# Kernel optimization log

Measured on AMD Instinct MI355X. Metric: run time of the kernel, lower is better.

## Reference

```python
import jax, jax.numpy as jnp
import numpy as np

N, E, B, F, H = 100000, 800000, 128, 128, 128
G = 5
INV_BN = np.float32(1.0 / np.sqrt(1.0 + 1e-5))  # eval BatchNorm, running_mean=0, running_var=1

_HEAD_SHAPES = [("norm_emb_g", (2*H,)), ("norm_emb_b", (2*H,)),
                ("fc1_W", (16, 2*H+1)), ("fc1_b", (16,)),
                ("bn1_g", (16,)), ("bn1_b", (16,)),
                ("fc2_W", (2, 2*H+3)), ("fc2_b", (2,)),
                ("fc3a_W", (4, 2*H+5)), ("fc3a_b", (4,)),
                ("fc3b_W", (5, 2*H+5)), ("fc3b_b", (5,)),
                ("normc_g", (2*H+5,)), ("normc_b", (2*H+5,))]


def setup_inputs() -> dict:
    key = jax.random.key(0)
    ks = jax.random.split(key, 64)
    p = lambda i, shape: jax.random.normal(ks[i], shape, jnp.float32) * 0.05
    inp = {
        "x": jax.random.normal(ks[0], (N, F), jnp.float32),
        "edge_index": jax.random.randint(ks[1], (2, E), 0, N, dtype=jnp.int32),
        "edge_direction": jax.random.randint(ks[2], (E,), 0, 2, dtype=jnp.int32),
        "batch": jnp.sort(jax.random.randint(ks[3], (N,), 0, B, dtype=jnp.int32)),
        "graph_feature": jax.random.normal(ks[4], (B, G), jnp.float32),
        "task": 1,
    }
    i = 5
    for pref in ("pre", "suc"):
        for l in range(3):
            inp[pref + "_Wl%d" % l] = p(i, (H, H)); i += 1
            inp[pref + "_bl%d" % l] = p(i, (H,)); i += 1
            inp[pref + "_Wr%d" % l] = p(i, (H, H)); i += 1
    for name, shape in _HEAD_SHAPES:
        inp[name] = p(i, shape); i += 1
    return inp


def reference(x, edge_index, edge_direction, batch, graph_feature, task,
              pre_Wl0, pre_bl0, pre_Wr0, pre_Wl1, pre_bl1, pre_Wr1, pre_Wl2, pre_bl2, pre_Wr2,
              suc_Wl0, suc_bl0, suc_Wr0, suc_Wl1, suc_bl1, suc_Wr1, suc_Wl2, suc_bl2, suc_Wr2,
              norm_emb_g, norm_emb_b, fc1_W, fc1_b, bn1_g, bn1_b, fc2_W, fc2_b,
              fc3a_W, fc3a_b, fc3b_W, fc3b_b, normc_g, normc_b):
    src, dst = edge_index[0], edge_index[1]
    pre_mask = (edge_direction == 0).astype(x.dtype)
    suc_mask = (edge_direction == 1).astype(x.dtype)

    def sage(h, mask, Wl, bl, Wr):
        # PyG SAGEConv: lin_l(scatter_mean(x[src] -> dst)) + lin_r(h); masked edges emulate
        # the edge_direction slicing without data-dependent shapes.
        msg = h[src] * mask[:, None]                              # [E, H]
        agg = jax.ops.segment_sum(msg, dst, num_segments=N)      # [N, H]
        cnt = jax.ops.segment_sum(mask, dst, num_segments=N)     # [N]
        mean = agg / jnp.maximum(cnt, 1.0)[:, None]
        return mean @ Wl.T + bl + h @ Wr.T

    bn = lambda v, g, b: g * (v * INV_BN) + b  # eval-mode BatchNorm1d after reset

    pre_x, suc_x = x, x
    for Wl, bl, Wr in ((pre_Wl0, pre_bl0, pre_Wr0), (pre_Wl1, pre_bl1, pre_Wr1), (pre_Wl2, pre_bl2, pre_Wr2)):
        pre_x = jax.nn.relu(sage(pre_x, pre_mask, Wl, bl, Wr))
    for Wl, bl, Wr in ((suc_Wl0, suc_bl0, suc_Wr0), (suc_Wl1, suc_bl1, suc_Wr1), (suc_Wl2, suc_bl2, suc_Wr2)):
        suc_x = jax.nn.relu(sage(suc_x, suc_mask, Wl, bl, Wr))

    comb = jnp.concatenate([pre_x, suc_x], axis=1)               # [N, 2H]
    gsum = jax.ops.segment_sum(comb, batch, num_segments=B)
    gcnt = jax.ops.segment_sum(jnp.ones((N,), comb.dtype), batch, num_segments=B)
    combined = bn(gsum / jnp.maximum(gcnt, 1.0)[:, None], norm_emb_g, norm_emb_b)  # [B, 2H]

    lev_lsb = graph_feature[:, -1:]
    nx3 = graph_feature[:, -3:]
    out1 = bn(jax.nn.relu(jnp.concatenate([combined, lev_lsb], 1) @ fc1_W.T + fc1_b), bn1_g, bn1_b)
    out2 = jax.nn.relu(jnp.concatenate([combined, nx3], 1) @ fc2_W.T + fc2_b)
    pred = jnp.argmax(out2, axis=1)

    wf1 = graph_feature[:, 2:3]
    wf2 = graph_feature[:, 1:2]
    x3 = bn(jnp.concatenate([combined, wf1, wf2, nx3], 1), normc_g, normc_b)
    b1 = x3 @ fc3a_W.T + fc3a_b                                  # [B, 4]
    b2 = x3 @ fc3b_W.T + fc3b_b                                  # [B, 5]
    out3 = jnp.concatenate([jnp.where((pred == 0)[:, None], b1, 0.0),
                            jnp.where((pred == 1)[:, None], b2, 0.0)], axis=1)  # [B, 9]
    return (out1, out2, out3)
```

## Files before the change

### kernel.cpp

```cpp
#include <hip/hip_runtime.h>

constexpr int kN = 100000;
constexpr int kNpad = 100096;
constexpr int kE = 800000;
constexpr int kB = 128;
constexpr int kBinsPerDir = 391;
constexpr int kNB = 782;
constexpr int kRep = 64;
constexpr int kCtrs = kNB * kRep;
constexpr int kTiles = kNpad / 256;
constexpr float kInvBN = 0.99999500003749968f;

constexpr int kXconvBlocks = 1024;
constexpr int kWprepBlocks = 192;
constexpr int kBincountBlocks = 782;
constexpr int kGstartBlocks = 391;
constexpr int kPrepBlocks = kXconvBlocks + kWprepBlocks + kBincountBlocks + kGstartBlocks;

typedef short s16x8 __attribute__((ext_vector_type(8)));
typedef float f32x4 __attribute__((ext_vector_type(4)));

__device__ inline ushort bf16rne(float f) {
  uint u = __builtin_bit_cast(uint, f);
  u += 0x7fffu + ((u >> 16) & 1u);
  return (ushort)(u >> 16);
}
__device__ inline float bflo(uint v) { return __builtin_bit_cast(float, v << 16); }
__device__ inline float bfhi(uint v) { return __builtin_bit_cast(float, v & 0xffff0000u); }
__device__ inline uint pack2(float a, float b) {
  return (uint)bf16rne(a) | ((uint)bf16rne(b) << 16);
}

struct WPtrs { const float* Wl[6]; const float* Wr[6]; };


__global__ __launch_bounds__(256) void prep_kernel(
    const float* __restrict__ x, ushort* __restrict__ xb,
    WPtrs p, ushort* __restrict__ Wb,
    const int* __restrict__ ei, const int* __restrict__ ed,
    int* __restrict__ bincnt,
    const int* __restrict__ batch, int* __restrict__ gstart) {
  int bi = blockIdx.x;
  int t = threadIdx.x;
  if (bi < kXconvBlocks) {
    constexpr int total = kNpad * 128 / 8;
    constexpr int stride = kXconvBlocks * 256;
    for (int i = bi * 256 + t; i < total; i += stride) {
      int i8 = i * 8;
      ushort4 r0, r1;
      if (i8 < kN * 128) {
        float4 v0 = *(const float4*)&x[i8];
        float4 v1 = *(const float4*)&x[i8 + 4];
        r0.x = bf16rne(v0.x); r0.y = bf16rne(v0.y); r0.z = bf16rne(v0.z); r0.w = bf16rne(v0.w);
        r1.x = bf16rne(v1.x); r1.y = bf16rne(v1.y); r1.z = bf16rne(v1.z); r1.w = bf16rne(v1.w);
      } else {
        r0.x = r0.y = r0.z = r0.w = 0;
        r1 = r0;
      }
      *(ushort4*)&xb[i8] = r0;
      *(ushort4*)&xb[i8 + 4] = r1;
    }
  } else if (bi < kXconvBlocks + kWprepBlocks) {
    int id4 = ((bi - kXconvBlocks) * 256 + t) * 4;
    int L = id4 >> 15;
    int o = (id4 >> 8) & 127, k = id4 & 255;
    const float* src = (k < 128) ? p.Wl[L] : p.Wr[L];
    float4 v = *(const float4*)&src[o * 128 + (k & 127)];
    ushort4 r;
    r.x = bf16rne(v.x); r.y = bf16rne(v.y); r.z = bf16rne(v.z); r.w = bf16rne(v.w);
    *(ushort4*)&Wb[id4] = r;
  } else if (bi < kXconvBlocks + kWprepBlocks + kBincountBlocks) {
    int e4 = ((bi - kXconvBlocks - kWprepBlocks) * 256 + t) * 4;
    if (e4 < kE) {
      int4 dv = *(const int4*)&ed[e4];
      int4 sv = *(const int4*)&ei[kE + e4];
      int dsts[4] = {sv.x, sv.y, sv.z, sv.w};
      int dirs[4] = {dv.x, dv.y, dv.z, dv.w};
#pragma unroll
      for (int k = 0; k < 4; ++k) {
        int e = e4 + k;
        if (e < kE) {
          int ctr = ((dirs[k] * kBinsPerDir + (dsts[k] >> 8)) << 6) | ((e >> 8) & 63);
          atomicAdd(&bincnt[ctr], 1);
        }
      }
    }
  } else {
    int n = (bi - kXconvBlocks - kWprepBlocks - kBincountBlocks) * 256 + t;
    if (n < kN) {
      int b = batch[n];
      int bprev = (n == 0) ? -1 : batch[n - 1];
      for (int g = bprev + 1; g <= b; ++g) gstart[g] = n;
      if (n == kN - 1)
        for (int g = b + 1; g <= kB; ++g) gstart[g] = kN;
    }
  }
}


__global__ __launch_bounds__(256) void scan1_kernel(const int* __restrict__ in,
                                                    int* __restrict__ out,
                                                    int* __restrict__ bsum, int M) {
  __shared__ int s[256];
  int t = threadIdx.x;
  int idx = blockIdx.x * 1024 + t * 4;
  int4 v = {0, 0, 0, 0};
  if (idx < M) v = *(const int4*)&in[idx];
  int tsum = v.x + v.y + v.z + v.w;
  s[t] = tsum;
  __syncthreads();
  for (int d = 1; d < 256; d <<= 1) {
    int tmp = (t >= d) ? s[t - d] : 0;
    __syncthreads();
    s[t] += tmp;
    __syncthreads();
  }
  int excl = s[t] - tsum;
  if (idx < M) {
    int4 o;
    o.x = excl; o.y = excl + v.x; o.z = o.y + v.y; o.w = o.z + v.z;
    *(int4*)&out[idx] = o;
  }
  if (t == 255) bsum[blockIdx.x] = s[255];
}

__global__ __launch_bounds__(256) void scan2_kernel(int* __restrict__ bsum, int nb,
                                                    int* __restrict__ ghist) {
  __shared__ int s[256];
  int t = threadIdx.x;
  if (t < 128) ghist[t] = 0;
  int v = (t < nb) ? bsum[t] : 0;
  s[t] = v;
  __syncthreads();
  for (int d = 1; d < 256; d <<= 1) {
    int tmp = (t >= d) ? s[t - d] : 0;
    __syncthreads();
    s[t] += tmp;
    __syncthreads();
  }
  if (t < nb) bsum[t] = s[t] - v;
}

__global__ __launch_bounds__(256) void scan3_kernel(int* __restrict__ out,
                                                    const int* __restrict__ bsum, int M,
                                                    int* __restrict__ bincur) {
  int idx = blockIdx.x * 1024 + threadIdx.x * 4;
  int add = bsum[blockIdx.x];
  if (idx < M) {
    int4 o = *(int4*)&out[idx];
    o.x += add; o.y += add; o.z += add; o.w += add;
    *(int4*)&out[idx] = o;
    int4 z = {0, 0, 0, 0};
    *(int4*)&bincur[idx] = z;
  }
}


__global__ __launch_bounds__(256) void binscatter_kernel(const int* __restrict__ ei,
                                                         const int* __restrict__ ed,
                                                         const int* __restrict__ binoff,
                                                         int* __restrict__ bincur,
                                                         uint* __restrict__ binbuf,
                                                         float* __restrict__ comb_raw) {
  int gid = blockIdx.x * 256 + threadIdx.x;
  if (gid < kB * 256 / 4) {
    float4 z = {0.f, 0.f, 0.f, 0.f};
    *(float4*)&comb_raw[gid * 4] = z;
  }
  if (gid >= kE) return;
  int dst = ei[kE + gid];
  int ctr = ((ed[gid] * kBinsPerDir + (dst >> 8)) << 6) | ((gid >> 8) & 63);
  int pos = atomicAdd(&bincur[ctr], 1);
  binbuf[binoff[ctr] + pos] = (uint)ei[gid] | ((uint)(dst & 255) << 17);
}

__global__ __launch_bounds__(256) void binfill_kernel(const uint* __restrict__ binbuf,
                                                      const int* __restrict__ binoff,
                                                      int* __restrict__ csr,
                                                      int* __restrict__ cnt,
                                                      int* __restrict__ off,
                                                      int* __restrict__ ghist,
                                                      int* __restrict__ blockbase,
                                                      uint* __restrict__ perm) {
  __shared__ int lcnt[256];
  __shared__ int ls[256];
  __shared__ int lpos[256];
  int b = blockIdx.x;
  int t = threadIdx.x;
  perm[b * 256 + t] = (uint)kN;
  int dir = (b >= kBinsPerDir) ? 1 : 0;
  int nodeBase = (b - dir * kBinsPerDir) << 8;
  int e0 = binoff[b * kRep];
  int e1 = (b == kNB - 1) ? kE : binoff[(b + 1) * kRep];
  lcnt[t] = 0;
  __syncthreads();
  for (int e = e0 + t; e < e1; e += 256) atomicAdd(&lcnt[binbuf[e] >> 17], 1);
  __syncthreads();
  int my = lcnt[t];
  ls[t] = my;
  __syncthreads();
  for (int d = 1; d < 256; d <<= 1) {
    int tmp = (t >= d) ? ls[t - d] : 0;
    __syncthreads();
    ls[t] += tmp;
    __syncthreads();
  }
  int excl = ls[t] - my;
  lpos[t] = e0 + excl;
  int node = nodeBase + t;
  if (node < kN) {
    int g = dir * kN + node;
    cnt[g] = my;
    off[g] = e0 + excl;
  }
  if (t < 64) lcnt[t] = 0;
  __syncthreads();
  if (node < kN) atomicAdd(&lcnt[min(my, 63)], 1);
  __syncthreads();
  if (t < 64) blockbase[b * 64 + t] = atomicAdd(&ghist[dir * 64 + t], lcnt[t]);
  __syncthreads();
  for (int e = e0 + t; e < e1; e += 256) {
    uint v = binbuf[e];
    int pos = atomicAdd(&lpos[v >> 17], 1);
    csr[pos] = (int)(v & 0x1FFFFu);
  }
}


__global__ __launch_bounds__(64) void dscan_kernel(int* __restrict__ ghist) {
  __shared__ int s[64];
  int t = threadIdx.x;
  for (int dir = 0; dir < 2; ++dir) {
    int v = ghist[dir * 64 + t];
    s[t] = v;
    __syncthreads();
    for (int d = 1; d < 64; d <<= 1) {
      int tmp = (t >= d) ? s[t - d] : 0;
      __syncthreads();
      s[t] += tmp;
      __syncthreads();
    }
    ghist[dir * 64 + t] = s[t] - v;
    __syncthreads();
  }
}

__global__ __launch_bounds__(256) void dscatter_kernel(const int* __restrict__ cnt,
                                                       const int* __restrict__ ghist,
                                                       const int* __restrict__ blockbase,
                                                       uint* __restrict__ perm) {
  __shared__ int h[64];
  int b = blockIdx.x;
  int t = threadIdx.x;
  int dir = (b >= kBinsPerDir) ? 1 : 0;
  int node = (b - dir * kBinsPerDir) * 256 + t;
  if (t < 64) h[t] = 0;
  __syncthreads();
  if (node < kN) {
    int bucket = min(cnt[dir * kN + node], 63);
    int r = atomicAdd(&h[bucket], 1);
    int pos = ghist[dir * 64 + bucket] + blockbase[b * 64 + bucket] + r;
    int ch = pos >> 4, wi = pos & 15;
    int q = ch / 391, rr = ch - q * 391;
    int pos2 = ((rr * 16 + q) << 4) | wi;
    perm[dir * kNpad + pos2] = (uint)node;
  }
}


__global__ __launch_bounds__(1024) void fused_layer_kernel(
    const ushort* __restrict__ hin0, const ushort* __restrict__ hin1,
    ushort* __restrict__ hout0, ushort* __restrict__ hout1,
    const ushort* __restrict__ Wb0, const ushort* __restrict__ Wb1,
    const float* __restrict__ bl0, const float* __restrict__ bl1,
    const int* __restrict__ off, const int* __restrict__ cnt,
    const int* __restrict__ csr, const uint* __restrict__ perm) {
  __shared__ ushort Wlds[128 * 256];

  const int dir = (blockIdx.x >= kTiles) ? 1 : 0;
  const int tile = blockIdx.x - dir * kTiles;
  const ushort* __restrict__ h = dir ? hin1 : hin0;
  ushort* __restrict__ outp = dir ? hout1 : hout0;
  const ushort* __restrict__ Wb = dir ? Wb1 : Wb0;
  const float* __restrict__ bl = dir ? bl1 : bl0;
  const uint* __restrict__ pp = perm + (size_t)dir * kNpad;
  const int dirbase = dir * kN;

  const int t = threadIdx.x;
  const int w = t >> 6;
  const int l = t & 63;
  const int lr = l & 15;
  const int lq = l >> 4;
  const int swz = lr & 7;

  const int node = (int)pp[tile * 256 + w * 16 + lr];
  int s = 0, c = 0;
  if (node < kN) {
    int bkt = dirbase + node;
    s = off[bkt];
    c = cnt[bkt];
  }
  s16x8 self[4];
#pragma unroll
  for (int q = 0; q < 4; ++q)
    self[q] = *(const s16x8*)(h + (size_t)node * 128 + q * 32 + lq * 8);

#pragma unroll
  for (int it = 0; it < 4; ++it) {
    int u = t + 1024 * it;
    int o = u >> 5, b = u & 31;
    uint4 v = *(const uint4*)(Wb + (size_t)u * 8);
    *(uint4*)((char*)Wlds + o * 512 + ((b ^ (o & 7)) << 4)) = v;
  }
  __syncthreads();

  float ga[32];
#pragma unroll
  for (int i = 0; i < 32; ++i) ga[i] = 0.f;
  {
    const ushort* hp = h + lq * 8;
    int e = 0;
    for (; e + 2 <= c; e += 2) {
      int s0 = csr[s + e];
      int s1 = csr[s + e + 1];
      const ushort* p0 = hp + (size_t)s0 * 128;
      const ushort* p1 = hp + (size_t)s1 * 128;
      uint4 va[4], vb[4];
#pragma unroll
      for (int q = 0; q < 4; ++q) va[q] = *(const uint4*)(p0 + q * 32);
#pragma unroll
      for (int q = 0; q < 4; ++q) vb[q] = *(const uint4*)(p1 + q * 32);
#pragma unroll
      for (int q = 0; q < 4; ++q) {
        ga[q * 8 + 0] += bflo(va[q].x) + bflo(vb[q].x);
        ga[q * 8 + 1] += bfhi(va[q].x) + bfhi(vb[q].x);
        ga[q * 8 + 2] += bflo(va[q].y) + bflo(vb[q].y);
        ga[q * 8 + 3] += bfhi(va[q].y) + bfhi(vb[q].y);
        ga[q * 8 + 4] += bflo(va[q].z) + bflo(vb[q].z);
        ga[q * 8 + 5] += bfhi(va[q].z) + bfhi(vb[q].z);
        ga[q * 8 + 6] += bflo(va[q].w) + bflo(vb[q].w);
        ga[q * 8 + 7] += bfhi(va[q].w) + bfhi(vb[q].w);
      }
    }
    if (e < c) {
      int s0 = csr[s + e];
      const ushort* p0 = hp + (size_t)s0 * 128;
      uint4 va[4];
#pragma unroll
      for (int q = 0; q < 4; ++q) va[q] = *(const uint4*)(p0 + q * 32);
#pragma unroll
      for (int q = 0; q < 4; ++q) {
        ga[q * 8 + 0] += bflo(va[q].x);
        ga[q * 8 + 1] += bfhi(va[q].x);
        ga[q * 8 + 2] += bflo(va[q].y);
        ga[q * 8 + 3] += bfhi(va[q].y);
        ga[q * 8 + 4] += bflo(va[q].z);
        ga[q * 8 + 5] += bfhi(va[q].z);
        ga[q * 8 + 6] += bflo(va[q].w);
        ga[q * 8 + 7] += bfhi(va[q].w);
      }
    }
  }
  float iv = 1.0f / fmaxf((float)c, 1.0f);
  s16x8 am[4];
#pragma unroll
  for (int q = 0; q < 4; ++q) {
    uint4 r;
    r.x = pack2(ga[q * 8 + 0] * iv, ga[q * 8 + 1] * iv);
    r.y = pack2(ga[q * 8 + 2] * iv, ga[q * 8 + 3] * iv);
    r.z = pack2(ga[q * 8 + 4] * iv, ga[q * 8 + 5] * iv);
    r.w = pack2(ga[q * 8 + 6] * iv, ga[q * 8 + 7] * iv);
    am[q] = __builtin_bit_cast(s16x8, r);
  }

  f32x4 acc[8];
#pragma unroll
  for (int j = 0; j < 8; ++j) acc[j] = {0.f, 0.f, 0.f, 0.f};

#pragma unroll
  for (int kk = 0; kk < 8; ++kk) {
    s16x8 a = (kk < 4) ? am[kk] : self[kk - 4];
    const int ks = (kk * 4 + lq) ^ swz;
#pragma unroll
    for (int j = 0; j < 8; ++j) {
      int o = j * 16 + lr;
      s16x8 wf = *(const s16x8*)((const char*)Wlds + o * 512 + (ks << 4));
      acc[j] = __builtin_amdgcn_mfma_f32_16x16x32_bf16(wf, a, acc[j], 0, 0, 0);
    }
  }

  if (node < kN) {
#pragma unroll
    for (int j = 0; j < 8; ++j) {
      int o = j * 16 + lq * 4;
      float4 bv = *(const float4*)(bl + o);
      ushort4 r;
      r.x = bf16rne(fmaxf(acc[j][0] + bv.x, 0.f));
      r.y = bf16rne(fmaxf(acc[j][1] + bv.y, 0.f));
      r.z = bf16rne(fmaxf(acc[j][2] + bv.z, 0.f));
      r.w = bf16rne(fmaxf(acc[j][3] + bv.w, 0.f));
      *(ushort4*)(outp + (size_t)node * 128 + o) = r;
    }
  }
}


__global__ __launch_bounds__(256) void pool_kernel(const ushort* __restrict__ hp0,
                                                   const ushort* __restrict__ hp1,
                                                   const int* __restrict__ gstart,
                                                   float* __restrict__ comb_raw) {
  __shared__ float part[4 * 128];
  int gb = blockIdx.x;
  int dir = gb >> 11;
  int rem = gb & 2047;
  int graph = rem >> 4;
  int chunk = rem & 15;
  const ushort* __restrict__ h = dir ? hp1 : hp0;
  int base = dir << 7;
  int t = threadIdx.x;
  int slice = t >> 6;
  int col = t & 63;
  int s = gstart[graph];
  int e = gstart[graph + 1];
  int len = e - s;
  int c0 = s + (int)((long long)len * chunk / 16);
  int c1 = s + (int)((long long)len * (chunk + 1) / 16);
  float ax = 0.f, ay = 0.f;
  for (int n = c0 + slice; n < c1; n += 4) {
    uint v = *(const uint*)(h + (size_t)n * 128 + col * 2);
    ax += bflo(v);
    ay += bfhi(v);
  }
  part[slice * 128 + col * 2] = ax;
  part[slice * 128 + col * 2 + 1] = ay;
  __syncthreads();
  if (t < 128) {
    float v = part[t] + part[128 + t] + part[256 + t] + part[384 + t];
    atomicAdd(&comb_raw[graph * 256 + base + t], v);
  }
}


__global__ __launch_bounds__(256) void head_kernel(
    const float* __restrict__ comb_raw, const int* __restrict__ gstart,
    const float* __restrict__ gf,
    const float* __restrict__ neg, const float* __restrict__ neb,
    const float* __restrict__ fc1W, const float* __restrict__ fc1b,
    const float* __restrict__ bn1g, const float* __restrict__ bn1b,
    const float* __restrict__ fc2W, const float* __restrict__ fc2b,
    const float* __restrict__ fc3aW, const float* __restrict__ fc3ab,
    const float* __restrict__ fc3bW, const float* __restrict__ fc3bb,
    const float* __restrict__ ncg, const float* __restrict__ ncb,
    float* __restrict__ out) {
  __shared__ float wlds[6979];
  __shared__ float comb[256];
  __shared__ float x3[261];
  __shared__ float r2s[2];

  const int b = blockIdx.x;
  const int t = threadIdx.x;

  for (int i = t; i < 4112; i += 256) wlds[i] = fc1W[i];
  for (int i = t; i < 518; i += 256) wlds[4112 + i] = fc2W[i];
  for (int i = t; i < 1044; i += 256) wlds[4630 + i] = fc3aW[i];
  for (int i = t; i < 1305; i += 256) wlds[5674 + i] = fc3bW[i];

  float cntf = fmaxf((float)(gstart[b + 1] - gstart[b]), 1.0f);
  if (t < 256) comb[t] = neg[t] * ((comb_raw[b * 256 + t] / cntf) * kInvBN) + neb[t];
  __syncthreads();

  float g1 = gf[b * 5 + 1], g2 = gf[b * 5 + 2], g3 = gf[b * 5 + 3], g4 = gf[b * 5 + 4];
  const int g = t >> 3, l8 = t & 7;

  {
    float p = 0.f;
    if (g < 16) {
      const float* w = &wlds[g * 257];
      for (int j = l8; j < 256; j += 8) p += comb[j] * w[j];
    } else if (g < 18) {
      const float* w = &wlds[4112 + (g - 16) * 259];
      for (int j = l8; j < 256; j += 8) p += comb[j] * w[j];
    }
    p += __shfl_xor(p, 1);
    p += __shfl_xor(p, 2);
    p += __shfl_xor(p, 4);
    if (l8 == 0) {
      if (g < 16) {
        float z = fmaxf(p + wlds[g * 257 + 256] * g4 + fc1b[g], 0.f);
        out[b * 16 + g] = bn1g[g] * (z * kInvBN) + bn1b[g];
      } else if (g < 18) {
        int o = g - 16;
        const float* w = &wlds[4112 + o * 259];
        float z = fmaxf(p + w[256] * g2 + w[257] * g3 + w[258] * g4 + fc2b[o], 0.f);
        out[2048 + b * 2 + o] = z;
        r2s[o] = z;
      }
    }
  }
  for (int j = t; j < 261; j += 256) {
    float v;
    if (j < 256) v = comb[j];
    else if (j == 256) v = g2;
    else if (j == 257) v = g1;
    else if (j == 258) v = g2;
    else if (j == 259) v = g3;
    else v = g4;
    x3[j] = ncg[j] * (v * kInvBN) + ncb[j];
  }
  __syncthreads();
  int pred = (r2s[1] > r2s[0]) ? 1 : 0;

  {
    float p = 0.f;
    if (g < 4) {
      const float* w = &wlds[4630 + g * 261];
      for (int j = l8; j < 261; j += 8) p += x3[j] * w[j];
    } else if (g < 9) {
      const float* w = &wlds[5674 + (g - 4) * 261];
      for (int j = l8; j < 261; j += 8) p += x3[j] * w[j];
    }
    p += __shfl_xor(p, 1);
    p += __shfl_xor(p, 2);
    p += __shfl_xor(p, 4);
    if (l8 == 0) {
      if (g < 4) {
        float v = p + fc3ab[g];
        out[2304 + b * 9 + g] = (pred == 0) ? v : 0.f;
      } else if (g < 9) {
        int o = g - 4;
        float v = p + fc3bb[o];
        out[2304 + b * 9 + 4 + o] = (pred == 1) ? v : 0.f;
      }
    }
  }
}


extern "C" void kernel_launch(void* const* d_in, const int* in_sizes, int n_in,
                              void* d_out, int out_size, void* d_ws, size_t ws_size,
                              hipStream_t stream) {
  (void)in_sizes; (void)n_in; (void)out_size; (void)ws_size;
  const float* x   = (const float*)d_in[0];
  const int* ei    = (const int*)d_in[1];
  const int* ed    = (const int*)d_in[2];
  const int* batch = (const int*)d_in[3];
  const float* gf  = (const float*)d_in[4];

  char* ws = (char*)d_ws;
  auto carve = [&](size_t bytes) -> void* {
    void* p = ws;
    ws += (bytes + 255) & ~(size_t)255;
    return p;
  };
  int* cnt        = (int*)carve(2 * kN * sizeof(int));
  int* off        = (int*)carve(2 * kN * sizeof(int));
  int* bincnt     = (int*)carve(kCtrs * sizeof(int));
  int* bincur     = (int*)carve((kCtrs + 4) * sizeof(int));
  int* binoff     = (int*)carve((kCtrs + 4) * sizeof(int));
  int* bsum       = (int*)carve(1024);
  int* gstart     = (int*)carve((kB + 1) * sizeof(int));
  int* ghist      = (int*)carve(128 * sizeof(int));
  int* blockbase  = (int*)carve(kNB * 64 * sizeof(int));
  uint* perm      = (uint*)carve(2 * kNpad * sizeof(uint));
  int* csr        = (int*)carve(kE * sizeof(int));
  uint* binbuf    = (uint*)carve(kE * sizeof(uint));
  float* comb_raw = (float*)carve(kB * 256 * sizeof(float));
  ushort* xb      = (ushort*)carve((size_t)kNpad * 128 * 2);
  ushort* p0      = (ushort*)carve((size_t)kNpad * 128 * 2);
  ushort* p1      = (ushort*)carve((size_t)kNpad * 128 * 2);
  ushort* s0      = (ushort*)carve((size_t)kNpad * 128 * 2);
  ushort* Wb      = (ushort*)carve(6 * 128 * 256 * 2);

  hipMemsetAsync(bincnt, 0, kCtrs * sizeof(int), stream);

  WPtrs wp;
  for (int L = 0; L < 6; ++L) {
    wp.Wl[L] = (const float*)d_in[6 + 3 * L];
    wp.Wr[L] = (const float*)d_in[6 + 3 * L + 2];
  }

  prep_kernel<<<kPrepBlocks, 256, 0, stream>>>(x, xb, wp, Wb, ei, ed, bincnt, batch, gstart);

  constexpr int NBScan = (kCtrs + 1023) / 1024;
  scan1_kernel<<<NBScan, 256, 0, stream>>>(bincnt, binoff, bsum, kCtrs);
  scan2_kernel<<<1, 256, 0, stream>>>(bsum, NBScan, ghist);
  scan3_kernel<<<NBScan, 256, 0, stream>>>(binoff, bsum, kCtrs, bincur);
  binscatter_kernel<<<(kE + 255) / 256, 256, 0, stream>>>(ei, ed, binoff, bincur, binbuf, comb_raw);
  binfill_kernel<<<kNB, 256, 0, stream>>>(binbuf, binoff, csr, cnt, off, ghist, blockbase, perm);
  dscan_kernel<<<1, 64, 0, stream>>>(ghist);
  dscatter_kernel<<<kNB, 256, 0, stream>>>(cnt, ghist, blockbase, perm);

  auto W = [&](int L) { return Wb + (size_t)L * 32768; };
  auto B = [&](int L) { return (const float*)d_in[6 + 3 * L + 1]; };

  fused_layer_kernel<<<2 * kTiles, 1024, 0, stream>>>(
      xb, xb, p0, s0, W(0), W(3), B(0), B(3), off, cnt, csr, perm);
  fused_layer_kernel<<<2 * kTiles, 1024, 0, stream>>>(
      p0, s0, p1, xb, W(1), W(4), B(1), B(4), off, cnt, csr, perm);
  fused_layer_kernel<<<2 * kTiles, 1024, 0, stream>>>(
      p1, xb, p0, s0, W(2), W(5), B(2), B(5), off, cnt, csr, perm);

  pool_kernel<<<2 * kB * 16, 256, 0, stream>>>(p0, s0, gstart, comb_raw);

  head_kernel<<<kB, 256, 0, stream>>>(
      comb_raw, gstart, gf,
      (const float*)d_in[24], (const float*)d_in[25],
      (const float*)d_in[26], (const float*)d_in[27],
      (const float*)d_in[28], (const float*)d_in[29],
      (const float*)d_in[30], (const float*)d_in[31],
      (const float*)d_in[32], (const float*)d_in[33],
      (const float*)d_in[34], (const float*)d_in[35],
      (const float*)d_in[36], (const float*)d_in[37],
      (float*)d_out);
}
```

Baseline: 358.0 us.

## Halve layer tile to 128 nodes, unroll neighbor gather by three, defer self load

The fused SAGE layer kernel now uses 512-thread blocks over 128-node tiles with launch bounds of 512 threads and 4 blocks per CU. The node permutation is re-interleaved to match the new tile count. The neighbor gather is unrolled to three edges per step to raise memory-level parallelism, and the self-feature load moves after aggregation to shorten register live ranges. The aim is better occupancy and latency hiding, at the cost of loading the 64KB weight tile into LDS twice as often per node.

Result: no change. 363.3 us (+1.5%).

```diff
diff --git a/kernel.cpp b/kernel.cpp
--- a/kernel.cpp
+++ b/kernel.cpp
@@ -8,7 +8,7 @@
 constexpr int kNB = 782;
 constexpr int kRep = 64;
 constexpr int kCtrs = kNB * kRep;
-constexpr int kTiles = kNpad / 256;
+constexpr int kTiles = kNpad / 128;
 constexpr float kInvBN = 0.99999500003749968f;
 
 constexpr int kXconvBlocks = 1024;
@@ -261,14 +261,14 @@
     int r = atomicAdd(&h[bucket], 1);
     int pos = ghist[dir * 64 + bucket] + blockbase[b * 64 + bucket] + r;
     int ch = pos >> 4, wi = pos & 15;
-    int q = ch / 391, rr = ch - q * 391;
-    int pos2 = ((rr * 16 + q) << 4) | wi;
+    int q = ch / 782, rr = ch - q * 782;
+    int pos2 = ((rr * 8 + q) << 4) | wi;
     perm[dir * kNpad + pos2] = (uint)node;
   }
 }
 
 
-__global__ __launch_bounds__(1024) void fused_layer_kernel(
+__global__ __launch_bounds__(512, 4) void fused_layer_kernel(
     const ushort* __restrict__ hin0, const ushort* __restrict__ hin1,
     ushort* __restrict__ hout0, ushort* __restrict__ hout1,
     const ushort* __restrict__ Wb0, const ushort* __restrict__ Wb1,
@@ -293,21 +293,17 @@
   const int lq = l >> 4;
   const int swz = lr & 7;
 
-  const int node = (int)pp[tile * 256 + w * 16 + lr];
+  const int node = (int)pp[tile * 128 + w * 16 + lr];
   int s = 0, c = 0;
   if (node < kN) {
     int bkt = dirbase + node;
     s = off[bkt];
     c = cnt[bkt];
   }
-  s16x8 self[4];
-#pragma unroll
-  for (int q = 0; q < 4; ++q)
-    self[q] = *(const s16x8*)(h + (size_t)node * 128 + q * 32 + lq * 8);
-
-#pragma unroll
-  for (int it = 0; it < 4; ++it) {
-    int u = t + 1024 * it;
+
+#pragma unroll
+  for (int it = 0; it < 8; ++it) {
+    int u = t + 512 * it;
     int o = u >> 5, b = u & 31;
     uint4 v = *(const uint4*)(Wb + (size_t)u * 8);
     *(uint4*)((char*)Wlds + o * 512 + ((b ^ (o & 7)) << 4)) = v;
@@ -320,45 +316,81 @@
   {
     const ushort* hp = h + lq * 8;
     int e = 0;
-    for (; e + 2 <= c; e += 2) {
+    for (; e + 3 <= c; e += 3) {
       int s0 = csr[s + e];
       int s1 = csr[s + e + 1];
-      const ushort* p0 = hp + (size_t)s0 * 128;
-      const ushort* p1 = hp + (size_t)s1 * 128;
-      uint4 va[4], vb[4];
-#pragma unroll
-      for (int q = 0; q < 4; ++q) va[q] = *(const uint4*)(p0 + q * 32);
-#pragma unroll
-      for (int q = 0; q < 4; ++q) vb[q] = *(const uint4*)(p1 + q * 32);
-#pragma unroll
-      for (int q = 0; q < 4; ++q) {
-        ga[q * 8 + 0] += bflo(va[q].x) + bflo(vb[q].x);
-        ga[q * 8 + 1] += bfhi(va[q].x) + bfhi(vb[q].x);
-        ga[q * 8 + 2] += bflo(va[q].y) + bflo(vb[q].y);
-        ga[q * 8 + 3] += bfhi(va[q].y) + bfhi(vb[q].y);
-        ga[q * 8 + 4] += bflo(va[q].z) + bflo(vb[q].z);
-        ga[q * 8 + 5] += bfhi(va[q].z) + bfhi(vb[q].z);
-        ga[q * 8 + 6] += bflo(va[q].w) + bflo(vb[q].w);
-        ga[q * 8 + 7] += bfhi(va[q].w) + bfhi(vb[q].w);
-      }
-    }
-    if (e < c) {
+      int s2 = csr[s + e + 2];
+      const ushort* q0 = hp + (size_t)s0 * 128;
+      const ushort* q1 = hp + (size_t)s1 * 128;
+      const ushort* q2 = hp + (size_t)s2 * 128;
+      uint4 a0 = *(const uint4*)(q0);
+      uint4 a1 = *(const uint4*)(q0 + 32);
+      uint4 a2 = *(const uint4*)(q0 + 64);
+      uint4 a3 = *(const uint4*)(q0 + 96);
+      uint4 b0 = *(const uint4*)(q1);
+      uint4 b1 = *(const uint4*)(q1 + 32);
+      uint4 b2 = *(const uint4*)(q1 + 64);
+      uint4 b3 = *(const uint4*)(q1 + 96);
+      uint4 c0 = *(const uint4*)(q2);
+      uint4 c1 = *(const uint4*)(q2 + 32);
+      uint4 c2 = *(const uint4*)(q2 + 64);
+      uint4 c3 = *(const uint4*)(q2 + 96);
+      ga[0] += bflo(a0.x) + bflo(b0.x) + bflo(c0.x);
+      ga[1] += bfhi(a0.x) + bfhi(b0.x) + bfhi(c0.x);
+      ga[2] += bflo(a0.y) + bflo(b0.y) + bflo(c0.y);
+      ga[3] += bfhi(a0.y) + bfhi(b0.y) + bfhi(c0.y);
+      ga[4] += bflo(a0.z) + bflo(b0.z) + bflo(c0.z);
+      ga[5] += bfhi(a0.z) + bfhi(b0.z) + bfhi(c0.z);
+      ga[6] += bflo(a0.w) + bflo(b0.w) + bflo(c0.w);
+      ga[7] += bfhi(a0.w) + bfhi(b0.w) + bfhi(c0.w);
+      ga[8] += bflo(a1.x) + bflo(b1.x) + bflo(c1.x);
+      ga[9] += bfhi(a1.x) + bfhi(b1.x) + bfhi(c1.x);
+      ga[10] += bflo(a1.y) + bflo(b1.y) + bflo(c1.y);
+      ga[11] += bfhi(a1.y) + bfhi(b1.y) + bfhi(c1.y);
+      ga[12] += bflo(a1.z) + bflo(b1.z) + bflo(c1.z);
+      ga[13] += bfhi(a1.z) + bfhi(b1.z) + bfhi(c1.z);
+      ga[14] += bflo(a1.w) + bflo(b1.w) + bflo(c1.w);
+      ga[15] += bfhi(a1.w) + bfhi(b1.w) + bfhi(c1.w);
+      ga[16] += bflo(a2.x) + bflo(b2.x) + bflo(c2.x);
+      ga[17] += bfhi(a2.x) + bfhi(b2.x) + bfhi(c2.x);
+      ga[18] += bflo(a2.y) + bflo(b2.y) + bflo(c2.y);
+      ga[19] += bfhi(a2.y) + bfhi(b2.y) + bfhi(c2.y);
+      ga[20] += bflo(a2.z) + bflo(b2.z) + bflo(c2.z);
+      ga[21] += bfhi(a2.z) + bfhi(b2.z) + bfhi(c2.z);
+      ga[22] += bflo(a2.w) + bflo(b2.w) + bflo(c2.w);
+      ga[23] += bfhi(a2.w) + bfhi(b2.w) + bfhi(c2.w);
+      ga[24] += bflo(a3.x) + bflo(b3.x) + bflo(c3.x);
+      ga[25] += bfhi(a3.x) + bfhi(b3.x) + bfhi(c3.x);
+      ga[26] += bflo(a3.y) + bflo(b3.y) + bflo(c3.y);
+      ga[27] += bfhi(a3.y) + bfhi(b3.y) + bfhi(c3.y);
+      ga[28] += bflo(a3.z) + bflo(b3.z) + bflo(c3.z);
+      ga[29] += bfhi(a3.z) + bfhi(b3.z) + bfhi(c3.z);
+      ga[30] += bflo(a3.w) + bflo(b3.w) + bflo(c3.w);
+      ga[31] += bfhi(a3.w) + bfhi(b3.w) + bfhi(c3.w);
+    }
+    for (; e < c; ++e) {
       int s0 = csr[s + e];
-      const ushort* p0 = hp + (size_t)s0 * 128;
-      uint4 va[4];
-#pragma unroll
-      for (int q = 0; q < 4; ++q) va[q] = *(const uint4*)(p0 + q * 32);
-#pragma unroll
-      for (int q = 0; q < 4; ++q) {
-        ga[q * 8 + 0] += bflo(va[q].x);
-        ga[q * 8 + 1] += bfhi(va[q].x);
-        ga[q * 8 + 2] += bflo(va[q].y);
-        ga[q * 8 + 3] += bfhi(va[q].y);
-        ga[q * 8 + 4] += bflo(va[q].z);
-        ga[q * 8 + 5] += bfhi(va[q].z);
-        ga[q * 8 + 6] += bflo(va[q].w);
-        ga[q * 8 + 7] += bfhi(va[q].w);
-      }
+      const ushort* q0 = hp + (size_t)s0 * 128;
+      uint4 a0 = *(const uint4*)(q0);
+      uint4 a1 = *(const uint4*)(q0 + 32);
+      uint4 a2 = *(const uint4*)(q0 + 64);
+      uint4 a3 = *(const uint4*)(q0 + 96);
+      ga[0] += bflo(a0.x); ga[1] += bfhi(a0.x);
+      ga[2] += bflo(a0.y); ga[3] += bfhi(a0.y);
+      ga[4] += bflo(a0.z); ga[5] += bfhi(a0.z);
+      ga[6] += bflo(a0.w); ga[7] += bfhi(a0.w);
+      ga[8] += bflo(a1.x); ga[9] += bfhi(a1.x);
+      ga[10] += bflo(a1.y); ga[11] += bfhi(a1.y);
+      ga[12] += bflo(a1.z); ga[13] += bfhi(a1.z);
+      ga[14] += bflo(a1.w); ga[15] += bfhi(a1.w);
+      ga[16] += bflo(a2.x); ga[17] += bfhi(a2.x);
+      ga[18] += bflo(a2.y); ga[19] += bfhi(a2.y);
+      ga[20] += bflo(a2.z); ga[21] += bfhi(a2.z);
+      ga[22] += bflo(a2.w); ga[23] += bfhi(a2.w);
+      ga[24] += bflo(a3.x); ga[25] += bfhi(a3.x);
+      ga[26] += bflo(a3.y); ga[27] += bfhi(a3.y);
+      ga[28] += bflo(a3.z); ga[29] += bfhi(a3.z);
+      ga[30] += bflo(a3.w); ga[31] += bfhi(a3.w);
     }
   }
   float iv = 1.0f / fmaxf((float)c, 1.0f);
@@ -372,6 +404,11 @@
     r.w = pack2(ga[q * 8 + 6] * iv, ga[q * 8 + 7] * iv);
     am[q] = __builtin_bit_cast(s16x8, r);
   }
+
+  s16x8 self[4];
+#pragma unroll
+  for (int q = 0; q < 4; ++q)
+    self[q] = *(const s16x8*)(h + (size_t)node * 128 + q * 32 + lq * 8);
 
   f32x4 acc[8];
 #pragma unroll
@@ -593,11 +630,11 @@
   auto W = [&](int L) { return Wb + (size_t)L * 32768; };
   auto B = [&](int L) { return (const float*)d_in[6 + 3 * L + 1]; };
 
-  fused_layer_kernel<<<2 * kTiles, 1024, 0, stream>>>(
+  fused_layer_kernel<<<2 * kTiles, 512, 0, stream>>>(
       xb, xb, p0, s0, W(0), W(3), B(0), B(3), off, cnt, csr, perm);
-  fused_layer_kernel<<<2 * kTiles, 1024, 0, stream>>>(
+  fused_layer_kernel<<<2 * kTiles, 512, 0, stream>>>(
       p0, s0, p1, xb, W(1), W(4), B(1), B(4), off, cnt, csr, perm);
-  fused_layer_kernel<<<2 * kTiles, 1024, 0, stream>>>(
+  fused_layer_kernel<<<2 * kTiles, 512, 0, stream>>>(
       p1, xb, p0, s0, W(2), W(5), B(2), B(5), off, cnt, csr, perm);
 
   pool_kernel<<<2 * kB * 16, 256, 0, stream>>>(p0, s0, gstart, comb_raw);
```
